# Optimization experiments

Measured on AMD Instinct MI355X. Metric: run time of the kernel, lower is better.

Reference implementation:

```python
import jax, jax.numpy as jnp
import numpy as np

EPS = 1e-5
K_EDE, T_EDE = 1.0, 0.1  # IR-Net EDE STE params (init values); forward is pure sign


def binq(x):
    # sign binarization (forward only)
    return jnp.sign(x)


def conv3x3(x, w):
    return jax.lax.conv_general_dilated(
        x, w, window_strides=(1, 1), padding=[(1, 1), (1, 1)],
        dimension_numbers=("NCHW", "OIHW", "NCHW"))


def batchnorm(x, g, b):
    # training-mode BN: batch statistics over (N,H,W), biased variance
    mu = x.mean(axis=(0, 2, 3), keepdims=True)
    var = x.var(axis=(0, 2, 3), keepdims=True)
    return (x - mu) * jax.lax.rsqrt(var + EPS) * g.reshape(1, -1, 1, 1) + b.reshape(1, -1, 1, 1)


def maxpool2(x):
    return jax.lax.reduce_window(x, -jnp.inf, jax.lax.max,
                                 (1, 1, 2, 2), (1, 1, 2, 2), "VALID")


def hardtanh(x):
    return jnp.clip(x, -1.0, 1.0)


def skd_ir_conv(xb, xr, w):
    # IR-Net style 1W1A conv: per-out-channel standardize weights, sign-binarize
    # weights and activations; real branch uses full-precision weights, no grad.
    m = w.mean(axis=(1, 2, 3), keepdims=True)
    s = w.std(axis=(1, 2, 3), keepdims=True, ddof=1)  # torch std is unbiased
    bw = binq((w - m) / s)
    yb = conv3x3(binq(xb), bw)
    yr = jax.lax.stop_gradient(conv3x3(xr, w))
    return yb, yr


def setup_inputs() -> dict:
    key = jax.random.key(0)
    ks = jax.random.split(key, 16)

    def conv_init(k, shape):
        fan = shape[2] * shape[3] * shape[0]
        return jax.random.normal(k, shape, jnp.float32) * np.sqrt(2.0 / fan)

    d = {
        "x": jax.random.normal(ks[0], (128, 3, 32, 32), jnp.float32),
        "w0": conv_init(ks[1], (128, 3, 3, 3)),
        "w1": conv_init(ks[2], (128, 128, 3, 3)),
        "w2": conv_init(ks[3], (256, 128, 3, 3)),
        "w3": conv_init(ks[4], (256, 256, 3, 3)),
        "w4": conv_init(ks[5], (512, 256, 3, 3)),
        "w5": conv_init(ks[6], (512, 512, 3, 3)),
        "fc_w": jax.random.normal(ks[7], (10, 512 * 4 * 4), jnp.float32) * 0.01,
        "fc_b": jnp.zeros((10,), jnp.float32),
    }
    chans = [128, 128, 256, 256, 512, 512]
    for i, c in enumerate(chans):
        d[f"g{i}"] = jnp.ones((c,), jnp.float32)
        d[f"b{i}"] = jnp.zeros((c,), jnp.float32)
    return d


def reference(x, w0, w1, w2, w3, w4, w5, fc_w, fc_b,
              g0, b0, g1, b1, g2, b2, g3, b3, g4, b4, g5, b5):
    x = hardtanh(batchnorm(conv3x3(x, w0), g0, b0))

    L1b, L1r = skd_ir_conv(x, jax.lax.stop_gradient(x), w1)
    L1b = hardtanh(batchnorm(maxpool2(L1b), g1, b1))
    L1r = jax.lax.stop_gradient(hardtanh(batchnorm(maxpool2(L1r), g1, b1)))

    L2b, L2r = skd_ir_conv(L1b, L1r, w2)
    L2b = hardtanh(batchnorm(L2b, g2, b2))
    L2r = jax.lax.stop_gradient(hardtanh(batchnorm(L2r, g2, b2)))

    L3b, L3r = skd_ir_conv(L2b, L2r, w3)
    L3b = hardtanh(batchnorm(maxpool2(L3b), g3, b3))
    L3r = jax.lax.stop_gradient(hardtanh(batchnorm(maxpool2(L3r), g3, b3)))

    L4b, L4r = skd_ir_conv(L3b, L3r, w4)
    L4b = hardtanh(batchnorm(L4b, g4, b4))
    L4r = jax.lax.stop_gradient(hardtanh(batchnorm(L4r, g4, b4)))

    L5b, L5r = skd_ir_conv(L4b, L4r, w5)
    L5b = hardtanh(batchnorm(maxpool2(L5b), g5, b5))
    L5r = jax.lax.stop_gradient(hardtanh(batchnorm(maxpool2(L5r), g5, b5)))

    penul = L5b.reshape(L5b.shape[0], -1)  # [B, 512*4*4]
    out = penul @ fc_w.T + fc_b
    return (out, penul, L1b, L1r, L2b, L2r, L3b, L3r, L4b, L4r, L5b, L5r)
```

## Files before the change

### kernel.cpp

```cpp
#include <hip/hip_runtime.h>


typedef unsigned short u16;
typedef __attribute__((ext_vector_type(8))) short short8;
typedef __attribute__((ext_vector_type(8))) unsigned short ushort8;
typedef __attribute__((ext_vector_type(4))) unsigned short ushort4v;
typedef __attribute__((ext_vector_type(4))) float float4v;

__device__ __forceinline__ float bf2f(u16 u) { return __uint_as_float(((unsigned)u) << 16); }
__device__ __forceinline__ u16 f2bf(float f) {
    unsigned u = __float_as_uint(f);
    return (u16)((u + 0x7FFFu + ((u >> 16) & 1u)) >> 16);
}
__device__ __forceinline__ u16 lo_bf(float y, u16 hi) {
    return f2bf(y - bf2f(hi));
}
__device__ __forceinline__ u16 signbf(float y) {
    return y > 0.f ? 0x3F80u : (y < 0.f ? 0xBF80u : 0u);
}

__global__ __launch_bounds__(256) void conv0_main(const float* __restrict__ x,
                                                  const float* __restrict__ w0,
                                                  float* __restrict__ out) {
    __shared__ float xt[306];
    __shared__ float wl[3456];
    const int t = threadIdx.x;
    const int n = blockIdx.x >> 5;
    const int h = blockIdx.x & 31;
    for (int i = t; i < 306; i += 256) xt[i] = 0.f;
    for (int i = t; i < 3456; i += 256) wl[i] = w0[i];
    __syncthreads();
    for (int i = t; i < 288; i += 256) {
        int ci = i / 96; int rr = (i / 32) % 3; int w = i & 31;
        int gh = h - 1 + rr;
        if (gh >= 0 && gh < 32)
            xt[(ci * 3 + rr) * 34 + w + 1] = x[((n * 3 + ci) * 32 + gh) * 32 + w];
    }
    __syncthreads();
    const int w = t & 31, cg = t >> 5;
    float xin[27];
#pragma unroll
    for (int ci = 0; ci < 3; ci++)
#pragma unroll
        for (int r = 0; r < 3; r++)
#pragma unroll
            for (int kw = 0; kw < 3; kw++)
                xin[(ci * 3 + r) * 3 + kw] = xt[(ci * 3 + r) * 34 + w + kw];
    float* o = out + ((size_t)(n * 1024 + h * 32 + w)) * 128 + cg * 16;
#pragma unroll
    for (int jq = 0; jq < 4; jq++) {
        float4v v;
#pragma unroll
        for (int jk = 0; jk < 4; jk++) {
            int co = cg * 16 + jq * 4 + jk;
            float a = 0.f;
#pragma unroll
            for (int e = 0; e < 27; e++) a += xin[e] * wl[co * 27 + e];
            v[jk] = a;
        }
        *(float4v*)(o + jq * 4) = v;
    }
}

__global__ __launch_bounds__(256) void stats0_kernel(const float* __restrict__ src,
                                                     float* __restrict__ st,
                                                     int C, int rows_per_block) {
    const int t = threadIdx.x;
    const int c = blockIdx.x * 64 + (t & 63);
    const int rg = t >> 6;
    const int r0 = blockIdx.y * rows_per_block;
    float s = 0.f, q = 0.f;
    for (int r = r0 + rg; r < r0 + rows_per_block; r += 4) {
        float v = src[(size_t)r * C + c];
        s += v;
        q += v * v;
    }
    __shared__ float Ls[256], Lq[256];
    Ls[t] = s; Lq[t] = q;
    __syncthreads();
    if (t < 64) {
        s = Ls[t] + Ls[t + 64] + Ls[t + 128] + Ls[t + 192];
        q = Lq[t] + Lq[t + 64] + Lq[t + 128] + Lq[t + 192];
        atomicAdd(&st[c], s);
        atomicAdd(&st[C + c], q);
    }
}

__global__ __launch_bounds__(256) void bn0_apply(const float* __restrict__ src,
                                                 const float* __restrict__ st,
                                                 const float* __restrict__ g,
                                                 const float* __restrict__ b,
                                                 u16* __restrict__ sg,
                                                 u16* __restrict__ hi,
                                                 u16* __restrict__ lo) {
    const int t = threadIdx.x;
    __shared__ float sc[128], sh[128];
    if (t < 128) {
        float mean = st[t] * (1.f / 131072.f);
        float var = fmaxf(st[128 + t] * (1.f / 131072.f) - mean * mean, 0.f);
        float scale = rsqrtf(var + 1e-5f) * g[t];
        sc[t] = scale;
        sh[t] = b[t] - mean * scale;
    }
    __syncthreads();
    size_t i = ((size_t)blockIdx.x * 256 + t) * 4;
    int c0 = (int)(i & 127);
    float4v v = *(const float4v*)(src + i);
    ushort4v hv, lv, sv;
#pragma unroll
    for (int k = 0; k < 4; k++) {
        float y = fminf(fmaxf(v[k] * sc[c0 + k] + sh[c0 + k], -1.f), 1.f);
        hv[k] = f2bf(y);
        lv[k] = lo_bf(y, hv[k]);
        sv[k] = signbf(y);
    }
    *(ushort4v*)(sg + i) = sv;
    *(ushort4v*)(hi + i) = hv;
    *(ushort4v*)(lo + i) = lv;
}

template <bool BIN>
__global__ __launch_bounds__(256) void prepack_kernel(const float* __restrict__ w,
                                                      u16* __restrict__ apk,
                                                      u16* __restrict__ apkLo,
                                                      int Cin, int Cout) {
    const int t = threadIdx.x, o = blockIdx.x;
    const int E = Cin * 9;
    float m = 0.f;
    if (BIN) {
        float s = 0.f;
        for (int e = t; e < E; e += 256) s += w[o * E + e];
        __shared__ float Ls[256];
        Ls[t] = s;
        __syncthreads();
        for (int stp = 128; stp > 0; stp >>= 1) {
            if (t < stp) Ls[t] += Ls[t + stp];
            __syncthreads();
        }
        m = Ls[0] / (float)E;
    }
    const int CC = Cin >> 5, COT = Cout >> 7;
    for (int e = t; e < E; e += 256) {
        int ci = e / 9, tap = e % 9;
        float raw = w[o * E + e];
        int idx = ((tap * CC + (ci >> 5)) * COT + (o >> 7)) * 4096 + (o & 127) * 32 + (ci & 31);
        if (BIN) {
            apk[idx] = signbf(raw - m);
        } else {
            u16 hi = f2bf(raw);
            apk[idx] = hi;
            apkLo[idx] = lo_bf(raw, hi);
        }
    }
}

template <bool POOL, bool BIN>
__global__ __launch_bounds__(512, 2) void conv_mfma_kernel(
    const u16* __restrict__ act, const u16* __restrict__ actLo,
    const u16* __restrict__ apk, const u16* __restrict__ apkLo,
    u16* __restrict__ out, u16* __restrict__ outLo,
    int Cin, int Cout, int H, int W) {
    const int HW = H * W;
    const int t = threadIdx.x;
    const int wave = t >> 6, lane = t & 63;
    const int l15 = lane & 15, quad = lane >> 4;
    const int wm = wave >> 1, wn = wave & 1;

    const int col0 = blockIdx.x * 128;
    const int cot = blockIdx.y;
    const int CC = Cin >> 5;
    const int COT = Cout >> 7;
    const bool two = (HW < 128);
    const int Wp = W + 2;
    const int nrows = two ? 2 * (H + 2) : (128 / W + 2);
    const int n0 = col0 / HW;
    const int h0 = two ? 0 : (col0 % HW) / W;

    __shared__ __align__(16) u16 BsH[2][8160];
    __shared__ __align__(16) u16 BsL[BIN ? 1 : 2][BIN ? 16 : 8160];

    int bbase[4], gcol[4];
#pragma unroll
    for (int ni = 0; ni < 4; ni++) {
        int c = wn * 64 + ni * 16 + l15;
        int g = col0 + c;
        int n = g / HW; int hw = g % HW; int h = hw / W; int w = hw % W;
        gcol[ni] = g;
        int rb = two ? ((n - n0) * (H + 2) + h) : (h - h0);
        bbase[ni] = (rb * Wp + w) * 40 + quad * 8;
    }

    const int bgroups = nrows * Wp * 4;
    int svalid[2]; size_t sgoff[2]; int sloff[2];
#pragma unroll
    for (int j = 0; j < 2; j++) {
        int idx = t + j * 512;
        svalid[j] = 0; sgoff[j] = 0; sloff[j] = 0;
        if (idx < bgroups) {
            int cig = idx & 3;
            int rest = idx >> 2;
            int wp = rest % Wp;
            int srow = rest / Wp;
            int n, gh;
            if (two) { n = n0 + srow / (H + 2); gh = srow % (H + 2) - 1; }
            else     { n = n0; gh = h0 + srow - 1; }
            int gw = wp - 1;
            sloff[j] = (srow * Wp + wp) * 40 + cig * 8;
            if (gh >= 0 && gh < H && gw >= 0 && gw < W) {
                svalid[j] = 2;
                sgoff[j] = ((size_t)(n * HW + gh * W + gw)) * Cin + cig * 8;
            } else {
                svalid[j] = 1;
            }
        }
    }

    float4v acc[2][4];
    const float4v zf = {0.f, 0.f, 0.f, 0.f};
#pragma unroll
    for (int mi = 0; mi < 2; mi++)
#pragma unroll
        for (int ni = 0; ni < 4; ni++) acc[mi][ni] = zf;

    const size_t tapstride = (size_t)CC * COT * 4096;
    const int arow0 = wm * 1024 + l15 * 32 + quad * 8;

    short8 ahP[2][2];
    short8 alP[2][2];
    short8 ah0N[2], al0N[2];
    short8 bhP[2][4];
    short8 blP[2][4];
    short8 svh[2], svl[2];
    const short8 z8 = {0, 0, 0, 0, 0, 0, 0, 0};

    {
        const u16* ab0 = apk + ((size_t)cot) * 4096;
        const u16* ab0L = apkLo + ((size_t)cot) * 4096;
#pragma unroll
        for (int mi = 0; mi < 2; mi++) {
            ahP[0][mi] = *(const short8*)(ab0 + arow0 + mi * 512);
            if (!BIN) alP[0][mi] = *(const short8*)(ab0L + arow0 + mi * 512);
        }
#pragma unroll
        for (int j = 0; j < 2; j++) {
            svh[j] = z8; svl[j] = z8;
            if (svalid[j] == 2) {
                svh[j] = *(const short8*)(act + sgoff[j]);
                if (!BIN) svl[j] = *(const short8*)(actLo + sgoff[j]);
            }
        }
#pragma unroll
        for (int j = 0; j < 2; j++) {
            if (svalid[j]) {
                *(short8*)&BsH[0][sloff[j]] = svh[j];
                if (!BIN) *(short8*)&BsL[0][sloff[j]] = svl[j];
            }
        }
        __syncthreads();
#pragma unroll
        for (int ni = 0; ni < 4; ni++) {
            bhP[0][ni] = *(const short8*)&BsH[0][bbase[ni]];
            if (!BIN) blP[0][ni] = *(const short8*)&BsL[0][bbase[ni]];
        }
    }

    for (int cc = 0; cc < CC; cc++) {
        const int cur = cc & 1, nx = cur ^ 1;
        const bool more = (cc + 1 < CC);
        const u16* ab = apk + ((size_t)(cc * COT + cot)) * 4096;
        const u16* abL = apkLo + ((size_t)(cc * COT + cot)) * 4096;

        if (more) {
            const size_t ccb = (size_t)(cc + 1) * 32;
#pragma unroll
            for (int j = 0; j < 2; j++) {
                svh[j] = z8; svl[j] = z8;
                if (svalid[j] == 2) {
                    svh[j] = *(const short8*)(act + sgoff[j] + ccb);
                    if (!BIN) svl[j] = *(const short8*)(actLo + sgoff[j] + ccb);
                }
            }
            const u16* abN = apk + ((size_t)((cc + 1) * COT + cot)) * 4096;
            const u16* abNL = apkLo + ((size_t)((cc + 1) * COT + cot)) * 4096;
#pragma unroll
            for (int mi = 0; mi < 2; mi++) {
                ah0N[mi] = *(const short8*)(abN + arow0 + mi * 512);
                if (!BIN) al0N[mi] = *(const short8*)(abNL + arow0 + mi * 512);
            }
        }

#pragma unroll
        for (int tap = 0; tap < 9; tap++) {
            const int curp = tap & 1, nxp = curp ^ 1;
            if (tap < 8) {
                const u16* at = ab + (size_t)(tap + 1) * tapstride;
#pragma unroll
                for (int mi = 0; mi < 2; mi++)
                    ahP[nxp][mi] = *(const short8*)(at + arow0 + mi * 512);
                if (!BIN) {
                    const u16* atL = abL + (size_t)(tap + 1) * tapstride;
#pragma unroll
                    for (int mi = 0; mi < 2; mi++)
                        alP[nxp][mi] = *(const short8*)(atL + arow0 + mi * 512);
                }
                const int kh1 = (tap + 1) / 3, kw1 = (tap + 1) % 3;
                const int boff1 = (kh1 * Wp + kw1) * 40;
#pragma unroll
                for (int ni = 0; ni < 4; ni++) {
                    bhP[nxp][ni] = *(const short8*)&BsH[cur][bbase[ni] + boff1];
                    if (!BIN) blP[nxp][ni] = *(const short8*)&BsL[cur][bbase[ni] + boff1];
                }
            }
            __builtin_amdgcn_sched_barrier(0);
            __builtin_amdgcn_s_setprio(1);
            if (BIN) {
#pragma unroll
                for (int mi = 0; mi < 2; mi++)
#pragma unroll
                    for (int ni = 0; ni < 4; ni++)
                        acc[mi][ni] = __builtin_amdgcn_mfma_f32_16x16x32_bf16(
                            ahP[curp][mi], bhP[curp][ni], acc[mi][ni], 0, 0, 0);
            } else {
#pragma unroll
                for (int mi = 0; mi < 2; mi++)
#pragma unroll
                    for (int ni = 0; ni < 4; ni++)
                        acc[mi][ni] = __builtin_amdgcn_mfma_f32_16x16x32_bf16(
                            ahP[curp][mi], bhP[curp][ni], acc[mi][ni], 0, 0, 0);
#pragma unroll
                for (int mi = 0; mi < 2; mi++)
#pragma unroll
                    for (int ni = 0; ni < 4; ni++)
                        acc[mi][ni] = __builtin_amdgcn_mfma_f32_16x16x32_bf16(
                            ahP[curp][mi], blP[curp][ni], acc[mi][ni], 0, 0, 0);
#pragma unroll
                for (int mi = 0; mi < 2; mi++)
#pragma unroll
                    for (int ni = 0; ni < 4; ni++)
                        acc[mi][ni] = __builtin_amdgcn_mfma_f32_16x16x32_bf16(
                            alP[curp][mi], bhP[curp][ni], acc[mi][ni], 0, 0, 0);
            }
            __builtin_amdgcn_s_setprio(0);
        }

        if (more) {
#pragma unroll
            for (int j = 0; j < 2; j++) {
                if (svalid[j]) {
                    *(short8*)&BsH[nx][sloff[j]] = svh[j];
                    if (!BIN) *(short8*)&BsL[nx][sloff[j]] = svl[j];
                }
            }
            __syncthreads();
#pragma unroll
            for (int mi = 0; mi < 2; mi++) {
                ahP[0][mi] = ah0N[mi];
                if (!BIN) alP[0][mi] = al0N[mi];
            }
#pragma unroll
            for (int ni = 0; ni < 4; ni++) {
                bhP[0][ni] = *(const short8*)&BsH[nx][bbase[ni]];
                if (!BIN) blP[0][ni] = *(const short8*)&BsL[nx][bbase[ni]];
            }
        }
    }

    const int cobase = cot * 128 + wm * 32 + quad * 4;
    auto store4 = [&](size_t off, float4v v) {
        if (BIN) {
            ushort4v r;
#pragma unroll
            for (int k = 0; k < 4; k++) r[k] = (u16)(short)(int)v[k];
            *(ushort4v*)(out + off) = r;
        } else {
            ushort4v hi, lo;
#pragma unroll
            for (int k = 0; k < 4; k++) {
                hi[k] = f2bf(v[k]);
                lo[k] = lo_bf(v[k], hi[k]);
            }
            *(ushort4v*)(out + off) = hi;
            *(ushort4v*)(outLo + off) = lo;
        }
    };

    if (!POOL) {
#pragma unroll
        for (int mi = 0; mi < 2; mi++)
#pragma unroll
            for (int ni = 0; ni < 4; ni++)
                store4((size_t)gcol[ni] * Cout + cobase + mi * 16, acc[mi][ni]);
    } else {
        const int pH = H >> 1, pW = W >> 1;
        if (W == 32) {
#pragma unroll
            for (int mi = 0; mi < 2; mi++)
#pragma unroll
                for (int nip = 0; nip < 2; nip++) {
                    float4v v;
#pragma unroll
                    for (int k = 0; k < 4; k++)
                        v[k] = fmaxf((float)acc[mi][nip][k], (float)acc[mi][nip + 2][k]);
#pragma unroll
                    for (int k = 0; k < 4; k++) {
                        float vv = v[k];
                        v[k] = fmaxf(vv, __shfl_xor(vv, 1, 64));
                    }
                    if ((l15 & 1) == 0) {
                        int pw = nip * 8 + (l15 >> 1);
                        int ph = (h0 >> 1) + wn;
                        int prow = (n0 * pH + ph) * pW + pw;
                        store4((size_t)prow * Cout + cobase + mi * 16, v);
                    }
                }
        } else if (W == 16) {
#pragma unroll
            for (int mi = 0; mi < 2; mi++)
#pragma unroll
                for (int nip = 0; nip < 4; nip += 2) {
                    float4v v;
#pragma unroll
                    for (int k = 0; k < 4; k++)
                        v[k] = fmaxf((float)acc[mi][nip][k], (float)acc[mi][nip + 1][k]);
#pragma unroll
                    for (int k = 0; k < 4; k++) {
                        float vv = v[k];
                        v[k] = fmaxf(vv, __shfl_xor(vv, 1, 64));
                    }
                    if ((l15 & 1) == 0) {
                        int pw = l15 >> 1;
                        int ph = (h0 + wn * 4 + nip) >> 1;
                        int prow = (n0 * pH + ph) * pW + pw;
                        store4((size_t)prow * Cout + cobase + mi * 16, v);
                    }
                }
        } else {
#pragma unroll
            for (int mi = 0; mi < 2; mi++)
#pragma unroll
                for (int ni = 0; ni < 4; ni++) {
                    float4v v = acc[mi][ni];
#pragma unroll
                    for (int k = 0; k < 4; k++) {
                        float vv = v[k];
                        vv = fmaxf(vv, __shfl_xor(vv, 1, 64));
                        v[k] = fmaxf(vv, __shfl_xor(vv, 8, 64));
                    }
                    if ((l15 & 9) == 0) {
                        int pw = l15 >> 1;
                        int ph = ni;
                        int n = n0 + wn;
                        int prow = (n * pH + ph) * pW + pw;
                        store4((size_t)prow * Cout + cobase + mi * 16, v);
                    }
                }
        }
    }
}

template <bool BIN>
__global__ __launch_bounds__(256) void stats_kernel(const u16* __restrict__ src,
                                                    const u16* __restrict__ srcLo,
                                                    float* __restrict__ st,
                                                    int C, int rows_per_block) {
    const int t = threadIdx.x;
    const int c = blockIdx.x * 64 + (t & 63);
    const int rg = t >> 6;
    const int r0 = blockIdx.y * rows_per_block;
    float s = 0.f, q = 0.f;
    for (int r = r0 + rg; r < r0 + rows_per_block; r += 4) {
        size_t i = (size_t)r * C + c;
        float v = BIN ? (float)(short)src[i] : (bf2f(src[i]) + bf2f(srcLo[i]));
        s += v;
        q += v * v;
    }
    __shared__ float Ls[256], Lq[256];
    Ls[t] = s; Lq[t] = q;
    __syncthreads();
    if (t < 64) {
        s = Ls[t] + Ls[t + 64] + Ls[t + 128] + Ls[t + 192];
        q = Lq[t] + Lq[t + 64] + Lq[t + 128] + Lq[t + 192];
        atomicAdd(&st[c], s);
        atomicAdd(&st[C + c], q);
    }
}

template <bool BIN>
__global__ __launch_bounds__(256) void bn_apply_kernel(const u16* __restrict__ src,
                                                       const u16* __restrict__ srcLo,
                                                       int C, int HW,
                                                       const float* __restrict__ st, float cntinv,
                                                       const float* __restrict__ g,
                                                       const float* __restrict__ b,
                                                       float* __restrict__ dout,
                                                       float* __restrict__ dout2,
                                                       u16* __restrict__ act,
                                                       u16* __restrict__ actLo,
                                                       int act_mode) {
    const int t = threadIdx.x;
    const int cl = t & 63, rl = t >> 6;
    const int c = blockIdx.y * 64 + cl;
    const float mean = st[c] * cntinv;
    float var = st[C + c] * cntinv - mean * mean;
    var = fmaxf(var, 0.f);
    const float scale = rsqrtf(var + 1e-5f) * g[c];
    const float shift = b[c] - mean * scale;
    __shared__ float T[64][65];
#pragma unroll
    for (int i = 0; i < 16; i++) {
        int rlocal = rl + i * 4;
        int row = blockIdx.x * 64 + rlocal;
        size_t idx = (size_t)row * C + c;
        float v = BIN ? (float)(short)src[idx] : (bf2f(src[idx]) + bf2f(srcLo[idx]));
        float y = fminf(fmaxf(v * scale + shift, -1.f), 1.f);
        if (act_mode == 1) {
            u16 hi = f2bf(y);
            act[idx] = hi;
            actLo[idx] = lo_bf(y, hi);
        } else if (act_mode == 2) {
            act[idx] = signbf(y);
        }
        T[rlocal][cl] = y;
    }
    __syncthreads();
#pragma unroll
    for (int i = 0; i < 16; i++) {
        int clocal = rl + i * 4;
        int cg = blockIdx.y * 64 + clocal;
        int rglob = blockIdx.x * 64 + cl;
        int n = rglob / HW, hw = rglob % HW;
        size_t o = ((size_t)n * C + cg) * HW + hw;
        float val = T[cl][clocal];
        dout[o] = val;
        if (dout2) dout2[o] = val;
    }
}

__global__ __launch_bounds__(256) void fc_kernel(const float* __restrict__ penul,
                                                 const float* __restrict__ fcw,
                                                 const float* __restrict__ fcb,
                                                 float* __restrict__ out) {
    const int t = threadIdx.x, n = blockIdx.x;
    float acc[10];
#pragma unroll
    for (int j = 0; j < 10; j++) acc[j] = 0.f;
    for (int i = t; i < 8192; i += 256) {
        float p = penul[n * 8192 + i];
#pragma unroll
        for (int j = 0; j < 10; j++) acc[j] += p * fcw[j * 8192 + i];
    }
    __shared__ float L[10][256];
#pragma unroll
    for (int j = 0; j < 10; j++) L[j][t] = acc[j];
    __syncthreads();
    for (int s = 128; s > 0; s >>= 1) {
        if (t < s) {
#pragma unroll
            for (int j = 0; j < 10; j++) L[j][t] += L[j][t + s];
        }
        __syncthreads();
    }
    if (t < 10) out[n * 10 + t] = L[t][0] + fcb[t];
}

extern "C" void kernel_launch(void* const* d_in, const int* in_sizes, int n_in,
                              void* d_out, int out_size, void* d_ws, size_t ws_size,
                              hipStream_t stream) {
    (void)in_sizes; (void)n_in; (void)out_size; (void)ws_size;

    const float* X = (const float*)d_in[0];
    const float* W0 = (const float*)d_in[1];
    const float* Wl[5] = {(const float*)d_in[2], (const float*)d_in[3], (const float*)d_in[4],
                          (const float*)d_in[5], (const float*)d_in[6]};
    const float* FCW = (const float*)d_in[7];
    const float* FCB = (const float*)d_in[8];
    const float* G[6]; const float* Bb[6];
    for (int i = 0; i < 6; i++) { G[i] = (const float*)d_in[9 + 2 * i]; Bb[i] = (const float*)d_in[10 + 2 * i]; }

    float* OUT = (float*)d_out;
    char* ws = (char*)d_ws;

    u16* apk   = (u16*)(ws);
    u16* apkLo = (u16*)(ws + 4718592);
    float* st0 = (float*)(ws + 9437184);
    float* stk = (float*)(ws + 9439232);
    u16* F     = (u16*)(ws + 9443328);
    u16* Flo   = (u16*)(ws + 26220544);
    u16* AB    = (u16*)(ws + 42997760);
    u16* AR    = (u16*)(ws + 59774976);
    u16* ARlo  = (u16*)(ws + 76552192);

    float* C0 = (float*)(ws + 9443328);
    u16* SG   = (u16*)(OUT + 26215680);
    u16* X0   = (u16*)(OUT + 9438464);
    u16* X0lo = (u16*)(OUT + 17827072);

    float* O_out = OUT;
    float* O_pen = OUT + 1280;
    float* O_L1b = OUT + 1049856;
    float* O_L1r = OUT + 5244160;
    float* O_L2b = OUT + 9438464;
    float* O_L2r = OUT + 17827072;
    float* O_L3b = OUT + 26215680;
    float* O_L3r = OUT + 28312832;
    float* O_L4b = OUT + 30409984;
    float* O_L4r = OUT + 34604288;
    float* O_L5b = OUT + 38798592;
    float* O_L5r = OUT + 39847168;

    conv0_main<<<4096, 256, 0, stream>>>(X, W0, C0);
    hipMemsetAsync(st0, 0, 2048, stream);
    stats0_kernel<<<dim3(2, 256), 256, 0, stream>>>(C0, st0, 128, 512);
    bn0_apply<<<16384, 256, 0, stream>>>(C0, st0, G[0], Bb[0], SG, X0, X0lo);

    struct Stage {
        const float* w; int Cin, Cout, H, W; bool pool;
        dim3 cgrid; dim3 sgrid; int srpb; dim3 bgrid; int bHW; float cntinv;
        float* db; float* dr;
    };
    const Stage S[5] = {
        {Wl[0], 128, 128, 32, 32, true,  dim3(1024, 1), dim3(2, 64), 512, dim3(512, 2), 256, 1.f / 32768.f, O_L1b, O_L1r},
        {Wl[1], 128, 256, 16, 16, false, dim3(256, 2),  dim3(4, 64), 512, dim3(512, 4), 256, 1.f / 32768.f, O_L2b, O_L2r},
        {Wl[2], 256, 256, 16, 16, true,  dim3(256, 2),  dim3(4, 16), 512, dim3(128, 4), 64,  1.f / 8192.f,  O_L3b, O_L3r},
        {Wl[3], 256, 512, 8, 8,   false, dim3(64, 4),   dim3(8, 16), 512, dim3(128, 8), 64,  1.f / 8192.f,  O_L4b, O_L4r},
        {Wl[4], 512, 512, 8, 8,   true,  dim3(64, 4),   dim3(8, 16), 128, dim3(32, 8),  16,  1.f / 2048.f,  O_L5b, O_L5r},
    };

    for (int k = 0; k < 5; k++) {
        const Stage& s = S[k];
        const u16* inB = (k == 0) ? SG : AB;
        const u16* inR = (k == 0) ? X0 : AR;
        const u16* inRlo = (k == 0) ? X0lo : ARlo;

        prepack_kernel<true><<<s.Cout, 256, 0, stream>>>(s.w, apk, nullptr, s.Cin, s.Cout);
        if (s.pool) conv_mfma_kernel<true, true><<<s.cgrid, 512, 0, stream>>>(inB, nullptr, apk, apk, F, nullptr, s.Cin, s.Cout, s.H, s.W);
        else        conv_mfma_kernel<false, true><<<s.cgrid, 512, 0, stream>>>(inB, nullptr, apk, apk, F, nullptr, s.Cin, s.Cout, s.H, s.W);
        hipMemsetAsync(stk, 0, 4096, stream);
        stats_kernel<true><<<s.sgrid, 256, 0, stream>>>(F, nullptr, stk, s.Cout, s.srpb);
        bn_apply_kernel<true><<<s.bgrid, 256, 0, stream>>>(F, nullptr, s.Cout, s.bHW, stk, s.cntinv,
                                                           G[k + 1], Bb[k + 1], s.db,
                                                           (k == 4) ? O_pen : nullptr,
                                                           AB, nullptr, (k == 4) ? 0 : 2);

        prepack_kernel<false><<<s.Cout, 256, 0, stream>>>(s.w, apk, apkLo, s.Cin, s.Cout);
        if (s.pool) conv_mfma_kernel<true, false><<<s.cgrid, 512, 0, stream>>>(inR, inRlo, apk, apkLo, F, Flo, s.Cin, s.Cout, s.H, s.W);
        else        conv_mfma_kernel<false, false><<<s.cgrid, 512, 0, stream>>>(inR, inRlo, apk, apkLo, F, Flo, s.Cin, s.Cout, s.H, s.W);
        hipMemsetAsync(stk, 0, 4096, stream);
        stats_kernel<false><<<s.sgrid, 256, 0, stream>>>(F, Flo, stk, s.Cout, s.srpb);
        bn_apply_kernel<false><<<s.bgrid, 256, 0, stream>>>(F, Flo, s.Cout, s.bHW, stk, s.cntinv,
                                                            G[k + 1], Bb[k + 1], s.dr, nullptr,
                                                            AR, ARlo, (k == 4) ? 0 : 1);
    }

    fc_kernel<<<128, 256, 0, stream>>>(O_pen, FCW, FCB, O_out);
}
```

Measured before the change: 1.381 ms.

## Reshape MFMA warp tiling to 2x4 waves with 64x32 per-wave tiles

```diff
diff --git a/kernel.cpp b/kernel.cpp
--- a/kernel.cpp
+++ b/kernel.cpp
@@ -164,7 +164,7 @@
     const int t = threadIdx.x;
     const int wave = t >> 6, lane = t & 63;
     const int l15 = lane & 15, quad = lane >> 4;
-    const int wm = wave >> 1, wn = wave & 1;
+    const int wm = wave & 1, wn = wave >> 1;
 
     const int col0 = blockIdx.x * 128;
     const int cot = blockIdx.y;
@@ -179,15 +179,25 @@
     __shared__ __align__(16) u16 BsH[2][8160];
     __shared__ __align__(16) u16 BsL[BIN ? 1 : 2][BIN ? 16 : 8160];
 
-    int bbase[4], gcol[4];
-#pragma unroll
-    for (int ni = 0; ni < 4; ni++) {
-        int c = wn * 64 + ni * 16 + l15;
-        int g = col0 + c;
-        int n = g / HW; int hw = g % HW; int h = hw / W; int w = hw % W;
-        gcol[ni] = g;
-        int rb = two ? ((n - n0) * (H + 2) + h) : (h - h0);
-        bbase[ni] = (rb * Wp + w) * 40 + quad * 8;
+    int bbase[2], gcol[2];
+    if (W == 32) {
+#pragma unroll
+        for (int ni = 0; ni < 2; ni++) {
+            int hl = ni * 2 + (l15 >> 3);
+            int w = wn * 8 + (l15 & 7);
+            gcol[ni] = n0 * HW + (h0 + hl) * W + w;
+            bbase[ni] = (hl * Wp + w) * 40 + quad * 8;
+        }
+    } else {
+#pragma unroll
+        for (int ni = 0; ni < 2; ni++) {
+            int c = wn * 32 + ni * 16 + l15;
+            int g = col0 + c;
+            int n = g / HW; int hw = g % HW; int h = hw / W; int w = hw % W;
+            gcol[ni] = g;
+            int rb = two ? ((n - n0) * (H + 2) + h) : (h - h0);
+            bbase[ni] = (rb * Wp + w) * 40 + quad * 8;
+        }
     }
 
     const int bgroups = nrows * Wp * 4;
@@ -215,21 +225,21 @@
         }
     }
 
-    float4v acc[2][4];
+    float4v acc[4][2];
     const float4v zf = {0.f, 0.f, 0.f, 0.f};
 #pragma unroll
-    for (int mi = 0; mi < 2; mi++)
-#pragma unroll
-        for (int ni = 0; ni < 4; ni++) acc[mi][ni] = zf;
+    for (int mi = 0; mi < 4; mi++)
+#pragma unroll
+        for (int ni = 0; ni < 2; ni++) acc[mi][ni] = zf;
 
     const size_t tapstride = (size_t)CC * COT * 4096;
-    const int arow0 = wm * 1024 + l15 * 32 + quad * 8;
-
-    short8 ahP[2][2];
-    short8 alP[2][2];
-    short8 ah0N[2], al0N[2];
-    short8 bhP[2][4];
-    short8 blP[2][4];
+    const int arow0 = wm * 2048 + l15 * 32 + quad * 8;
+
+    short8 ahP[2][4];
+    short8 alP[2][4];
+    short8 ah0N[4], al0N[4];
+    short8 bhP[2][2];
+    short8 blP[2][2];
     short8 svh[2], svl[2];
     const short8 z8 = {0, 0, 0, 0, 0, 0, 0, 0};
 
@@ -237,7 +247,7 @@
         const u16* ab0 = apk + ((size_t)cot) * 4096;
         const u16* ab0L = apkLo + ((size_t)cot) * 4096;
 #pragma unroll
-        for (int mi = 0; mi < 2; mi++) {
+        for (int mi = 0; mi < 4; mi++) {
             ahP[0][mi] = *(const short8*)(ab0 + arow0 + mi * 512);
             if (!BIN) alP[0][mi] = *(const short8*)(ab0L + arow0 + mi * 512);
         }
@@ -258,7 +268,7 @@
         }
         __syncthreads();
 #pragma unroll
-        for (int ni = 0; ni < 4; ni++) {
+        for (int ni = 0; ni < 2; ni++) {
             bhP[0][ni] = *(const short8*)&BsH[0][bbase[ni]];
             if (!BIN) blP[0][ni] = *(const short8*)&BsL[0][bbase[ni]];
         }
@@ -283,7 +293,7 @@
             const u16* abN = apk + ((size_t)((cc + 1) * COT + cot)) * 4096;
             const u16* abNL = apkLo + ((size_t)((cc + 1) * COT + cot)) * 4096;
 #pragma unroll
-            for (int mi = 0; mi < 2; mi++) {
+            for (int mi = 0; mi < 4; mi++) {
                 ah0N[mi] = *(const short8*)(abN + arow0 + mi * 512);
                 if (!BIN) al0N[mi] = *(const short8*)(abNL + arow0 + mi * 512);
             }
@@ -295,18 +305,18 @@
             if (tap < 8) {
                 const u16* at = ab + (size_t)(tap + 1) * tapstride;
 #pragma unroll
-                for (int mi = 0; mi < 2; mi++)
+                for (int mi = 0; mi < 4; mi++)
                     ahP[nxp][mi] = *(const short8*)(at + arow0 + mi * 512);
                 if (!BIN) {
                     const u16* atL = abL + (size_t)(tap + 1) * tapstride;
 #pragma unroll
-                    for (int mi = 0; mi < 2; mi++)
+                    for (int mi = 0; mi < 4; mi++)
                         alP[nxp][mi] = *(const short8*)(atL + arow0 + mi * 512);
                 }
                 const int kh1 = (tap + 1) / 3, kw1 = (tap + 1) % 3;
                 const int boff1 = (kh1 * Wp + kw1) * 40;
 #pragma unroll
-                for (int ni = 0; ni < 4; ni++) {
+                for (int ni = 0; ni < 2; ni++) {
                     bhP[nxp][ni] = *(const short8*)&BsH[cur][bbase[ni] + boff1];
                     if (!BIN) blP[nxp][ni] = *(const short8*)&BsL[cur][bbase[ni] + boff1];
                 }
@@ -315,28 +325,28 @@
             __builtin_amdgcn_s_setprio(1);
             if (BIN) {
 #pragma unroll
-                for (int mi = 0; mi < 2; mi++)
-#pragma unroll
-                    for (int ni = 0; ni < 4; ni++)
+                for (int mi = 0; mi < 4; mi++)
+#pragma unroll
+                    for (int ni = 0; ni < 2; ni++)
                         acc[mi][ni] = __builtin_amdgcn_mfma_f32_16x16x32_bf16(
                             ahP[curp][mi], bhP[curp][ni], acc[mi][ni], 0, 0, 0);
             } else {
 #pragma unroll
-                for (int mi = 0; mi < 2; mi++)
-#pragma unroll
-                    for (int ni = 0; ni < 4; ni++)
+                for (int mi = 0; mi < 4; mi++)
+#pragma unroll
+                    for (int ni = 0; ni < 2; ni++)
                         acc[mi][ni] = __builtin_amdgcn_mfma_f32_16x16x32_bf16(
                             ahP[curp][mi], bhP[curp][ni], acc[mi][ni], 0, 0, 0);
 #pragma unroll
-                for (int mi = 0; mi < 2; mi++)
-#pragma unroll
-                    for (int ni = 0; ni < 4; ni++)
+                for (int mi = 0; mi < 4; mi++)
+#pragma unroll
+                    for (int ni = 0; ni < 2; ni++)
                         acc[mi][ni] = __builtin_amdgcn_mfma_f32_16x16x32_bf16(
                             ahP[curp][mi], blP[curp][ni], acc[mi][ni], 0, 0, 0);
 #pragma unroll
-                for (int mi = 0; mi < 2; mi++)
-#pragma unroll
-                    for (int ni = 0; ni < 4; ni++)
+                for (int mi = 0; mi < 4; mi++)
+#pragma unroll
+                    for (int ni = 0; ni < 2; ni++)
                         acc[mi][ni] = __builtin_amdgcn_mfma_f32_16x16x32_bf16(
                             alP[curp][mi], bhP[curp][ni], acc[mi][ni], 0, 0, 0);
             }
@@ -353,19 +363,19 @@
             }
             __syncthreads();
 #pragma unroll
-            for (int mi = 0; mi < 2; mi++) {
+            for (int mi = 0; mi < 4; mi++) {
                 ahP[0][mi] = ah0N[mi];
                 if (!BIN) alP[0][mi] = al0N[mi];
             }
 #pragma unroll
-            for (int ni = 0; ni < 4; ni++) {
+            for (int ni = 0; ni < 2; ni++) {
                 bhP[0][ni] = *(const short8*)&BsH[nx][bbase[ni]];
                 if (!BIN) blP[0][ni] = *(const short8*)&BsL[nx][bbase[ni]];
             }
         }
     }
 
-    const int cobase = cot * 128 + wm * 32 + quad * 4;
+    const int cobase = cot * 128 + wm * 64 + quad * 4;
     auto store4 = [&](size_t off, float4v v) {
         if (BIN) {
             ushort4v r;
@@ -386,70 +396,66 @@
 
     if (!POOL) {
 #pragma unroll
-        for (int mi = 0; mi < 2; mi++)
-#pragma unroll
-            for (int ni = 0; ni < 4; ni++)
+        for (int mi = 0; mi < 4; mi++)
+#pragma unroll
+            for (int ni = 0; ni < 2; ni++)
                 store4((size_t)gcol[ni] * Cout + cobase + mi * 16, acc[mi][ni]);
     } else {
         const int pH = H >> 1, pW = W >> 1;
         if (W == 32) {
 #pragma unroll
-            for (int mi = 0; mi < 2; mi++)
-#pragma unroll
-                for (int nip = 0; nip < 2; nip++) {
-                    float4v v;
-#pragma unroll
-                    for (int k = 0; k < 4; k++)
-                        v[k] = fmaxf((float)acc[mi][nip][k], (float)acc[mi][nip + 2][k]);
+            for (int mi = 0; mi < 4; mi++)
+#pragma unroll
+                for (int ni = 0; ni < 2; ni++) {
+                    float4v v = acc[mi][ni];
 #pragma unroll
                     for (int k = 0; k < 4; k++) {
                         float vv = v[k];
+                        vv = fmaxf(vv, __shfl_xor(vv, 8, 64));
                         v[k] = fmaxf(vv, __shfl_xor(vv, 1, 64));
                     }
-                    if ((l15 & 1) == 0) {
-                        int pw = nip * 8 + (l15 >> 1);
-                        int ph = (h0 >> 1) + wn;
+                    if ((l15 & 9) == 0) {
+                        int pw = wn * 4 + ((l15 & 7) >> 1);
+                        int ph = (h0 >> 1) + ni;
                         int prow = (n0 * pH + ph) * pW + pw;
                         store4((size_t)prow * Cout + cobase + mi * 16, v);
                     }
                 }
         } else if (W == 16) {
 #pragma unroll
-            for (int mi = 0; mi < 2; mi++)
-#pragma unroll
-                for (int nip = 0; nip < 4; nip += 2) {
-                    float4v v;
-#pragma unroll
-                    for (int k = 0; k < 4; k++)
-                        v[k] = fmaxf((float)acc[mi][nip][k], (float)acc[mi][nip + 1][k]);
+            for (int mi = 0; mi < 4; mi++) {
+                float4v v;
+#pragma unroll
+                for (int k = 0; k < 4; k++)
+                    v[k] = fmaxf((float)acc[mi][0][k], (float)acc[mi][1][k]);
+#pragma unroll
+                for (int k = 0; k < 4; k++) {
+                    float vv = v[k];
+                    v[k] = fmaxf(vv, __shfl_xor(vv, 1, 64));
+                }
+                if ((l15 & 1) == 0) {
+                    int pw = l15 >> 1;
+                    int ph = (h0 >> 1) + wn;
+                    int prow = (n0 * pH + ph) * pW + pw;
+                    store4((size_t)prow * Cout + cobase + mi * 16, v);
+                }
+            }
+        } else {
+#pragma unroll
+            for (int mi = 0; mi < 4; mi++)
+#pragma unroll
+                for (int ni = 0; ni < 2; ni++) {
+                    float4v v = acc[mi][ni];
 #pragma unroll
                     for (int k = 0; k < 4; k++) {
                         float vv = v[k];
+                        vv = fmaxf(vv, __shfl_xor(vv, 8, 64));
                         v[k] = fmaxf(vv, __shfl_xor(vv, 1, 64));
                     }
-                    if ((l15 & 1) == 0) {
-                        int pw = l15 >> 1;
-                        int ph = (h0 + wn * 4 + nip) >> 1;
-                        int prow = (n0 * pH + ph) * pW + pw;
-                        store4((size_t)prow * Cout + cobase + mi * 16, v);
-                    }
-                }
-        } else {
-#pragma unroll
-            for (int mi = 0; mi < 2; mi++)
-#pragma unroll
-                for (int ni = 0; ni < 4; ni++) {
-                    float4v v = acc[mi][ni];
-#pragma unroll
-                    for (int k = 0; k < 4; k++) {
-                        float vv = v[k];
-                        vv = fmaxf(vv, __shfl_xor(vv, 1, 64));
-                        v[k] = fmaxf(vv, __shfl_xor(vv, 8, 64));
-                    }
                     if ((l15 & 9) == 0) {
-                        int pw = l15 >> 1;
-                        int ph = ni;
-                        int n = n0 + wn;
+                        int pw = (l15 & 7) >> 1;
+                        int ph = (wn & 1) * 2 + ni;
+                        int n = n0 + (wn >> 1);
                         int prow = (n * pH + ph) * pW + pw;
                         store4((size_t)prow * Cout + cobase + mi * 16, v);
                     }
```

New measurement: 1.723 ms. +24.8%, slower.

## Fuse batchnorm statistics into conv epilogues and drop stats kernels

Applied to the files above, without the earlier changes.

```diff
diff --git a/kernel.cpp b/kernel.cpp
--- a/kernel.cpp
+++ b/kernel.cpp
@@ -21,14 +21,17 @@
 
 __global__ __launch_bounds__(256) void conv0_main(const float* __restrict__ x,
                                                   const float* __restrict__ w0,
-                                                  float* __restrict__ out) {
+                                                  float* __restrict__ out,
+                                                  float* __restrict__ st0) {
     __shared__ float xt[306];
     __shared__ float wl[3456];
+    __shared__ float S0[128], Q0[128];
     const int t = threadIdx.x;
     const int n = blockIdx.x >> 5;
     const int h = blockIdx.x & 31;
     for (int i = t; i < 306; i += 256) xt[i] = 0.f;
     for (int i = t; i < 3456; i += 256) wl[i] = w0[i];
+    if (t < 128) { S0[t] = 0.f; Q0[t] = 0.f; }
     __syncthreads();
     for (int i = t; i < 288; i += 256) {
         int ci = i / 96; int rr = (i / 32) % 3; int w = i & 31;
@@ -59,30 +62,24 @@
             v[jk] = a;
         }
         *(float4v*)(o + jq * 4) = v;
-    }
-}
-
-__global__ __launch_bounds__(256) void stats0_kernel(const float* __restrict__ src,
-                                                     float* __restrict__ st,
-                                                     int C, int rows_per_block) {
-    const int t = threadIdx.x;
-    const int c = blockIdx.x * 64 + (t & 63);
-    const int rg = t >> 6;
-    const int r0 = blockIdx.y * rows_per_block;
-    float s = 0.f, q = 0.f;
-    for (int r = r0 + rg; r < r0 + rows_per_block; r += 4) {
-        float v = src[(size_t)r * C + c];
-        s += v;
-        q += v * v;
-    }
-    __shared__ float Ls[256], Lq[256];
-    Ls[t] = s; Lq[t] = q;
+#pragma unroll
+        for (int jk = 0; jk < 4; jk++) {
+            float s = v[jk], q = v[jk] * v[jk];
+            s += __shfl_xor(s, 1, 64);  q += __shfl_xor(q, 1, 64);
+            s += __shfl_xor(s, 2, 64);  q += __shfl_xor(q, 2, 64);
+            s += __shfl_xor(s, 4, 64);  q += __shfl_xor(q, 4, 64);
+            s += __shfl_xor(s, 8, 64);  q += __shfl_xor(q, 8, 64);
+            s += __shfl_xor(s, 16, 64); q += __shfl_xor(q, 16, 64);
+            if ((t & 31) == 0) {
+                atomicAdd(&S0[cg * 16 + jq * 4 + jk], s);
+                atomicAdd(&Q0[cg * 16 + jq * 4 + jk], q);
+            }
+        }
+    }
     __syncthreads();
-    if (t < 64) {
-        s = Ls[t] + Ls[t + 64] + Ls[t + 128] + Ls[t + 192];
-        q = Lq[t] + Lq[t + 64] + Lq[t + 128] + Lq[t + 192];
-        atomicAdd(&st[c], s);
-        atomicAdd(&st[C + c], q);
+    if (t < 128) {
+        atomicAdd(&st0[t], S0[t]);
+        atomicAdd(&st0[128 + t], Q0[t]);
     }
 }
 
@@ -123,8 +120,12 @@
 __global__ __launch_bounds__(256) void prepack_kernel(const float* __restrict__ w,
                                                       u16* __restrict__ apk,
                                                       u16* __restrict__ apkLo,
-                                                      int Cin, int Cout) {
+                                                      int Cin, int Cout,
+                                                      float* __restrict__ stz) {
     const int t = threadIdx.x, o = blockIdx.x;
+    if (o == 0) {
+        stz[t] = 0.f; stz[256 + t] = 0.f; stz[512 + t] = 0.f; stz[768 + t] = 0.f;
+    }
     const int E = Cin * 9;
     float m = 0.f;
     if (BIN) {
@@ -159,7 +160,8 @@
     const u16* __restrict__ act, const u16* __restrict__ actLo,
     const u16* __restrict__ apk, const u16* __restrict__ apkLo,
     u16* __restrict__ out, u16* __restrict__ outLo,
-    int Cin, int Cout, int H, int W) {
+    int Cin, int Cout, int H, int W,
+    float* __restrict__ st) {
     const int HW = H * W;
     const int t = threadIdx.x;
     const int wave = t >> 6, lane = t & 63;
@@ -178,6 +180,7 @@
 
     __shared__ __align__(16) u16 BsH[2][8160];
     __shared__ __align__(16) u16 BsL[BIN ? 1 : 2][BIN ? 16 : 8160];
+    __shared__ float Sred[128], Qred[128];
 
     int bbase[4], gcol[4];
 #pragma unroll
@@ -256,6 +259,7 @@
                 if (!BIN) *(short8*)&BsL[0][sloff[j]] = svl[j];
             }
         }
+        if (t < 128) { Sred[t] = 0.f; Qred[t] = 0.f; }
         __syncthreads();
 #pragma unroll
         for (int ni = 0; ni < 4; ni++) {
@@ -366,7 +370,14 @@
     }
 
     const int cobase = cot * 128 + wm * 32 + quad * 4;
-    auto store4 = [&](size_t off, float4v v) {
+    float cs[2][4] = {{0.f, 0.f, 0.f, 0.f}, {0.f, 0.f, 0.f, 0.f}};
+    float cq[2][4] = {{0.f, 0.f, 0.f, 0.f}, {0.f, 0.f, 0.f, 0.f}};
+    auto store4 = [&](size_t off, float4v v, int mi) {
+#pragma unroll
+        for (int k = 0; k < 4; k++) {
+            cs[mi][k] += v[k];
+            cq[mi][k] += v[k] * v[k];
+        }
         if (BIN) {
             ushort4v r;
 #pragma unroll
@@ -389,7 +400,7 @@
         for (int mi = 0; mi < 2; mi++)
 #pragma unroll
             for (int ni = 0; ni < 4; ni++)
-                store4((size_t)gcol[ni] * Cout + cobase + mi * 16, acc[mi][ni]);
+                store4((size_t)gcol[ni] * Cout + cobase + mi * 16, acc[mi][ni], mi);
     } else {
         const int pH = H >> 1, pW = W >> 1;
         if (W == 32) {
@@ -410,7 +421,7 @@
                         int pw = nip * 8 + (l15 >> 1);
                         int ph = (h0 >> 1) + wn;
                         int prow = (n0 * pH + ph) * pW + pw;
-                        store4((size_t)prow * Cout + cobase + mi * 16, v);
+                        store4((size_t)prow * Cout + cobase + mi * 16, v, mi);
                     }
                 }
         } else if (W == 16) {
@@ -431,7 +442,7 @@
                         int pw = l15 >> 1;
                         int ph = (h0 + wn * 4 + nip) >> 1;
                         int prow = (n0 * pH + ph) * pW + pw;
-                        store4((size_t)prow * Cout + cobase + mi * 16, v);
+                        store4((size_t)prow * Cout + cobase + mi * 16, v, mi);
                     }
                 }
         } else {
@@ -451,37 +462,31 @@
                         int ph = ni;
                         int n = n0 + wn;
                         int prow = (n * pH + ph) * pW + pw;
-                        store4((size_t)prow * Cout + cobase + mi * 16, v);
+                        store4((size_t)prow * Cout + cobase + mi * 16, v, mi);
                     }
                 }
         }
     }
-}
-
-template <bool BIN>
-__global__ __launch_bounds__(256) void stats_kernel(const u16* __restrict__ src,
-                                                    const u16* __restrict__ srcLo,
-                                                    float* __restrict__ st,
-                                                    int C, int rows_per_block) {
-    const int t = threadIdx.x;
-    const int c = blockIdx.x * 64 + (t & 63);
-    const int rg = t >> 6;
-    const int r0 = blockIdx.y * rows_per_block;
-    float s = 0.f, q = 0.f;
-    for (int r = r0 + rg; r < r0 + rows_per_block; r += 4) {
-        size_t i = (size_t)r * C + c;
-        float v = BIN ? (float)(short)src[i] : (bf2f(src[i]) + bf2f(srcLo[i]));
-        s += v;
-        q += v * v;
-    }
-    __shared__ float Ls[256], Lq[256];
-    Ls[t] = s; Lq[t] = q;
+
+#pragma unroll
+    for (int mi = 0; mi < 2; mi++)
+#pragma unroll
+        for (int k = 0; k < 4; k++) {
+            float s = cs[mi][k], q = cq[mi][k];
+            s += __shfl_xor(s, 1, 64);  q += __shfl_xor(q, 1, 64);
+            s += __shfl_xor(s, 2, 64);  q += __shfl_xor(q, 2, 64);
+            s += __shfl_xor(s, 4, 64);  q += __shfl_xor(q, 4, 64);
+            s += __shfl_xor(s, 8, 64);  q += __shfl_xor(q, 8, 64);
+            if (l15 == 0) {
+                int cl = wm * 32 + mi * 16 + quad * 4 + k;
+                atomicAdd(&Sred[cl], s);
+                atomicAdd(&Qred[cl], q);
+            }
+        }
     __syncthreads();
-    if (t < 64) {
-        s = Ls[t] + Ls[t + 64] + Ls[t + 128] + Ls[t + 192];
-        q = Lq[t] + Lq[t + 64] + Lq[t + 128] + Lq[t + 192];
-        atomicAdd(&st[c], s);
-        atomicAdd(&st[C + c], q);
+    if (t < 128) {
+        atomicAdd(&st[cot * 128 + t], Sred[t]);
+        atomicAdd(&st[Cout + cot * 128 + t], Qred[t]);
     }
 }
 
@@ -608,22 +613,21 @@
     float* O_L5b = OUT + 38798592;
     float* O_L5r = OUT + 39847168;
 
-    conv0_main<<<4096, 256, 0, stream>>>(X, W0, C0);
     hipMemsetAsync(st0, 0, 2048, stream);
-    stats0_kernel<<<dim3(2, 256), 256, 0, stream>>>(C0, st0, 128, 512);
+    conv0_main<<<4096, 256, 0, stream>>>(X, W0, C0, st0);
     bn0_apply<<<16384, 256, 0, stream>>>(C0, st0, G[0], Bb[0], SG, X0, X0lo);
 
     struct Stage {
         const float* w; int Cin, Cout, H, W; bool pool;
-        dim3 cgrid; dim3 sgrid; int srpb; dim3 bgrid; int bHW; float cntinv;
+        dim3 cgrid; dim3 bgrid; int bHW; float cntinv;
         float* db; float* dr;
     };
     const Stage S[5] = {
-        {Wl[0], 128, 128, 32, 32, true,  dim3(1024, 1), dim3(2, 64), 512, dim3(512, 2), 256, 1.f / 32768.f, O_L1b, O_L1r},
-        {Wl[1], 128, 256, 16, 16, false, dim3(256, 2),  dim3(4, 64), 512, dim3(512, 4), 256, 1.f / 32768.f, O_L2b, O_L2r},
-        {Wl[2], 256, 256, 16, 16, true,  dim3(256, 2),  dim3(4, 16), 512, dim3(128, 4), 64,  1.f / 8192.f,  O_L3b, O_L3r},
-        {Wl[3], 256, 512, 8, 8,   false, dim3(64, 4),   dim3(8, 16), 512, dim3(128, 8), 64,  1.f / 8192.f,  O_L4b, O_L4r},
-        {Wl[4], 512, 512, 8, 8,   true,  dim3(64, 4),   dim3(8, 16), 128, dim3(32, 8),  16,  1.f / 2048.f,  O_L5b, O_L5r},
+        {Wl[0], 128, 128, 32, 32, true,  dim3(1024, 1), dim3(512, 2), 256, 1.f / 32768.f, O_L1b, O_L1r},
+        {Wl[1], 128, 256, 16, 16, false, dim3(256, 2),  dim3(512, 4), 256, 1.f / 32768.f, O_L2b, O_L2r},
+        {Wl[2], 256, 256, 16, 16, true,  dim3(256, 2),  dim3(128, 4), 64,  1.f / 8192.f,  O_L3b, O_L3r},
+        {Wl[3], 256, 512, 8, 8,   false, dim3(64, 4),   dim3(128, 8), 64,  1.f / 8192.f,  O_L4b, O_L4r},
+        {Wl[4], 512, 512, 8, 8,   true,  dim3(64, 4),   dim3(32, 8),  16,  1.f / 2048.f,  O_L5b, O_L5r},
     };
 
     for (int k = 0; k < 5; k++) {
@@ -632,21 +636,17 @@
         const u16* inR = (k == 0) ? X0 : AR;
         const u16* inRlo = (k == 0) ? X0lo : ARlo;
 
-        prepack_kernel<true><<<s.Cout, 256, 0, stream>>>(s.w, apk, nullptr, s.Cin, s.Cout);
-        if (s.pool) conv_mfma_kernel<true, true><<<s.cgrid, 512, 0, stream>>>(inB, nullptr, apk, apk, F, nullptr, s.Cin, s.Cout, s.H, s.W);
-        else        conv_mfma_kernel<false, true><<<s.cgrid, 512, 0, stream>>>(inB, nullptr, apk, apk, F, nullptr, s.Cin, s.Cout, s.H, s.W);
-        hipMemsetAsync(stk, 0, 4096, stream);
-        stats_kernel<true><<<s.sgrid, 256, 0, stream>>>(F, nullptr, stk, s.Cout, s.srpb);
+        prepack_kernel<true><<<s.Cout, 256, 0, stream>>>(s.w, apk, nullptr, s.Cin, s.Cout, stk);
+        if (s.pool) conv_mfma_kernel<true, true><<<s.cgrid, 512, 0, stream>>>(inB, nullptr, apk, apk, F, nullptr, s.Cin, s.Cout, s.H, s.W, stk);
+        else        conv_mfma_kernel<false, true><<<s.cgrid, 512, 0, stream>>>(inB, nullptr, apk, apk, F, nullptr, s.Cin, s.Cout, s.H, s.W, stk);
         bn_apply_kernel<true><<<s.bgrid, 256, 0, stream>>>(F, nullptr, s.Cout, s.bHW, stk, s.cntinv,
                                                            G[k + 1], Bb[k + 1], s.db,
                                                            (k == 4) ? O_pen : nullptr,
                                                            AB, nullptr, (k == 4) ? 0 : 2);
 
-        prepack_kernel<false><<<s.Cout, 256, 0, stream>>>(s.w, apk, apkLo, s.Cin, s.Cout);
-        if (s.pool) conv_mfma_kernel<true, false><<<s.cgrid, 512, 0, stream>>>(inR, inRlo, apk, apkLo, F, Flo, s.Cin, s.Cout, s.H, s.W);
-        else        conv_mfma_kernel<false, false><<<s.cgrid, 512, 0, stream>>>(inR, inRlo, apk, apkLo, F, Flo, s.Cin, s.Cout, s.H, s.W);
-        hipMemsetAsync(stk, 0, 4096, stream);
-        stats_kernel<false><<<s.sgrid, 256, 0, stream>>>(F, Flo, stk, s.Cout, s.srpb);
+        prepack_kernel<false><<<s.Cout, 256, 0, stream>>>(s.w, apk, apkLo, s.Cin, s.Cout, stk);
+        if (s.pool) conv_mfma_kernel<true, false><<<s.cgrid, 512, 0, stream>>>(inR, inRlo, apk, apkLo, F, Flo, s.Cin, s.Cout, s.H, s.W, stk);
+        else        conv_mfma_kernel<false, false><<<s.cgrid, 512, 0, stream>>>(inR, inRlo, apk, apkLo, F, Flo, s.Cin, s.Cout, s.H, s.W, stk);
         bn_apply_kernel<false><<<s.bgrid, 256, 0, stream>>>(F, Flo, s.Cout, s.bHW, stk, s.cntinv,
                                                             G[k + 1], Bb[k + 1], s.dr, nullptr,
                                                             AR, ARlo, (k == 4) ? 0 : 1);
```

Measured after the change: 1.191 ms. -13.8%, faster.
